# Kernel tuning notes

Hardware: AMD Instinct MI355X
Metric: run time of the kernel (lower is better)

Reference implementation:

```python
import jax, jax.numpy as jnp
import numpy as np

N = 20000      # nodes
E = 320000     # edges (avg degree 16)
F_IN = 32      # raw node feature dim
D = 128        # GNN_EMBEDDING_DIM = out_channels per head
HEADS = 4
RNN_H = 128    # RNN_HIDDEN_DIM
NEG_SLOPE = 0.2


def setup_inputs() -> dict:
    key = jax.random.key(0)
    ks = jax.random.split(key, 16)
    s = 0.05
    return {
        "node_features": jax.random.normal(ks[0], (N, F_IN), jnp.float32),
        "hidden_state": jax.random.normal(ks[1], (1, RNN_H), jnp.float32),
        "W_enc": jax.random.normal(ks[2], (F_IN, D), jnp.float32) * s,
        "b_enc": jax.random.normal(ks[3], (D,), jnp.float32) * s,
        "W_l": jax.random.normal(ks[4], (D, HEADS * D), jnp.float32) * s,
        "b_l": jax.random.normal(ks[5], (HEADS * D,), jnp.float32) * s,
        "W_r": jax.random.normal(ks[6], (D, HEADS * D), jnp.float32) * s,
        "b_r": jax.random.normal(ks[7], (HEADS * D,), jnp.float32) * s,
        "att": jax.random.normal(ks[8], (HEADS, D), jnp.float32) * s,
        "gat_bias": jax.random.normal(ks[9], (D,), jnp.float32) * s,
        "W_ih": jax.random.normal(ks[10], (3 * RNN_H, D), jnp.float32) * s,
        "W_hh": jax.random.normal(ks[11], (3 * RNN_H, RNN_H), jnp.float32) * s,
        "b_ih": jax.random.normal(ks[12], (3 * RNN_H,), jnp.float32) * s,
        "b_hh": jax.random.normal(ks[13], (3 * RNN_H,), jnp.float32) * s,
        "edge_index": jax.random.randint(ks[14], (2, E), 0, N, jnp.int32),
    }


def reference(node_features, hidden_state, W_enc, b_enc, W_l, b_l, W_r, b_r,
              att, gat_bias, W_ih, W_hh, b_ih, b_hh, edge_index):
    n = node_features.shape[0]
    # node encoder + ReLU
    h = jax.nn.relu(node_features @ W_enc + b_enc)                 # [N, D]

    # GATv2Conv (heads=4, concat=False), add_self_loops=True, eval (no dropout)
    loop = jnp.arange(n, dtype=edge_index.dtype)
    src = jnp.concatenate([edge_index[0], loop])                   # source j
    dst = jnp.concatenate([edge_index[1], loop])                   # target i

    xl = (h @ W_l + b_l).reshape(n, HEADS, D)                      # source proj
    xr = (h @ W_r + b_r).reshape(n, HEADS, D)                      # target proj

    e = jax.nn.leaky_relu(xl[src] + xr[dst], NEG_SLOPE)            # [Et, H, C]
    logits = jnp.einsum('ehc,hc->eh', e, att)                      # [Et, H]

    # segment softmax over incoming edges of each target node
    m = jax.ops.segment_max(logits, dst, num_segments=n)           # [N, H]
    m = jnp.where(jnp.isfinite(m), m, 0.0)
    p = jnp.exp(logits - m[dst])
    denom = jax.ops.segment_sum(p, dst, num_segments=n)
    alpha = p / jnp.maximum(denom[dst], 1e-16)                     # [Et, H]

    out = jax.ops.segment_sum(xl[src] * alpha[..., None], dst, num_segments=n)
    gat = out.mean(axis=1) + gat_bias                              # [N, D]

    # agent node 0 -> GRUCell (torch gate order: r, z, n)
    x = gat[0:1]                                                   # [1, D]
    gi = x @ W_ih.T + b_ih
    gh = hidden_state @ W_hh.T + b_hh
    i_r, i_z, i_n = jnp.split(gi, 3, axis=-1)
    h_r, h_z, h_n = jnp.split(gh, 3, axis=-1)
    r = jax.nn.sigmoid(i_r + h_r)
    z = jax.nn.sigmoid(i_z + h_z)
    ng = jnp.tanh(i_n + r * h_n)
    return (1.0 - z) * ng + z * hidden_state                       # [1, RNN_H]
```

## Files before the change

kernel.cpp:

```cpp
#include <hip/hip_runtime.h>


#define NBLK 40
#define NXL  16
#define XRB  16
#define GHB  24
#define FINB 36
#define SLOTS3 8
#define CAP  40
#define FLAGMAGIC 0x5A5A0000u

struct KP {
    const int* ei; int E;
    const float *nf, *W_enc, *b_enc, *W_l, *b_l, *W_r, *b_r, *att, *gat_bias,
                *hprev, *W_ih, *W_hh, *b_ih, *b_hh;
    unsigned *scnt;
    unsigned *xlflag;
    unsigned *xrflag;
    unsigned *gatflag;
    unsigned *giflag;
    int      *sslots;
    float *xr0;
    float *ghw;
    float *giw;
    float *gat;
    float *lgpart;
    float *xlw;
    float *out;
};

__device__ __forceinline__ unsigned pollFlag(unsigned* p) {
    for (long it = 0; it < 50000000L; ++it) {
        unsigned v = atomicOr(p, 0u);
        if ((v & 0xFFFF0000u) == FLAGMAGIC) return v & 0xFFFFu;
        __builtin_amdgcn_s_sleep(2);
    }
    return 0u;
}

__global__ __launch_bounds__(256) void k_all(KP p)
{
    __shared__ __align__(16) float buf[14720];
    __shared__ float aux[512];
    __shared__ int   iaux[128];
    const int t = threadIdx.x, b = blockIdx.x;

    if (t == 0) iaux[0] = 0;
    __syncthreads();
    if ((p.E & 3) == 0) {
        int nv = p.E >> 2;
        int per = (nv + NBLK - 1) / NBLK;
        int lo = b * per, hi = min(lo + per, nv);
        const int4* d4 = (const int4*)(p.ei + p.E);
        for (int it0 = lo; it0 < hi; it0 += 2048) {
            int4 v[8];
            #pragma unroll
            for (int k = 0; k < 8; ++k) {
                int i = it0 + t + k * 256;
                v[k] = (i < hi) ? d4[i] : make_int4(1, 1, 1, 1);
            }
            #pragma unroll
            for (int k = 0; k < 8; ++k) {
                int i = it0 + t + k * 256;
                if (v[k].x == 0 || v[k].y == 0 || v[k].z == 0 || v[k].w == 0) {
                    #pragma unroll
                    for (int c = 0; c < 4; ++c) {
                        if ((&v[k].x)[c] == 0) {
                            int q = atomicAdd(&iaux[0], 1);
                            if (q < SLOTS3) iaux[8 + q] = p.ei[4 * (long)i + c];
                        }
                    }
                }
            }
        }
    } else {
        int per = (p.E + NBLK - 1) / NBLK;
        long lo = (long)b * per, hi = lo + per; if (hi > p.E) hi = p.E;
        for (long i = lo + t; i < hi; i += 256) {
            if (p.ei[p.E + i] == 0) {
                int q = atomicAdd(&iaux[0], 1);
                if (q < SLOTS3) iaux[8 + q] = p.ei[i];
            }
        }
    }
    __syncthreads();
    int myc = min(iaux[0], SLOTS3);
    if (t < myc) p.sslots[b * SLOTS3 + t] = iaux[8 + t];
    __syncthreads();
    __threadfence();
    if (t == 0) atomicExch(&p.scnt[b * 16], FLAGMAGIC | (unsigned)myc);
    if (b > FINB) return;

    if (b >= XRB && b < GHB) {
        int q = b - XRB;
        for (int idx = t; idx < 2048; idx += 256) {
            int row = idx >> 4, f4 = idx & 15;
            ((float4*)buf)[idx] = *(const float4*)(p.W_r + (long)row * 512 + q * 64 + f4 * 4);
        }
        for (int idx = t; idx < 1024; idx += 256)
            ((float4*)(buf + 8192))[idx] = ((const float4*)p.W_enc)[idx];
        if (t < 32) aux[384 + t] = p.nf[t];
        __syncthreads();
        if (t < 128) {
            float a0 = 0, a1 = 0, a2 = 0, a3 = 0;
            #pragma unroll
            for (int k = 0; k < 32; k += 4) {
                a0 += aux[384 + k]     * buf[8192 + k * 128 + t];
                a1 += aux[384 + k + 1] * buf[8192 + (k + 1) * 128 + t];
                a2 += aux[384 + k + 2] * buf[8192 + (k + 2) * 128 + t];
                a3 += aux[384 + k + 3] * buf[8192 + (k + 3) * 128 + t];
            }
            aux[t] = fmaxf(a0 + a1 + a2 + a3 + p.b_enc[t], 0.f);
        }
        __syncthreads();
        {
            int jq = t & 63, ch = t >> 6;
            float a = 0.f;
            #pragma unroll 8
            for (int cc = 0; cc < 32; ++cc) {
                int c = ch * 32 + cc;
                a += aux[c] * buf[c * 64 + jq];
            }
            aux[128 + ch * 64 + jq] = a;
        }
        __syncthreads();
        if (t < 64) {
            int j = q * 64 + t;
            p.xr0[j] = aux[128 + t] + aux[192 + t] + aux[256 + t] + aux[320 + t]
                     + p.b_r[j];
        }
        __syncthreads();
        __threadfence();
        if (t == 0) atomicExch(&p.xrflag[q * 16], FLAGMAGIC | 1u);
        return;
    }

    if (b >= GHB && b < FINB) {
        int g = b - GHB;
        for (int idx = t; idx < 1024; idx += 256) {
            int row = idx >> 5, f4 = idx & 31;
            ((float4*)buf)[idx] = *(const float4*)(p.W_hh + (long)(g * 32 + row) * 128 + f4 * 4);
            ((float4*)(buf + 4096))[idx] = *(const float4*)(p.W_ih + (long)(g * 32 + row) * 128 + f4 * 4);
        }
        if (t < 128) aux[t] = p.hprev[t];
        __syncthreads();
        {
            int w = t >> 6, l = t & 63;
            #pragma unroll
            for (int i = 0; i < 8; ++i) {
                int rl = w * 8 + i;
                float pp = buf[rl * 128 + 2 * l] * aux[2 * l]
                         + buf[rl * 128 + 2 * l + 1] * aux[2 * l + 1];
                #pragma unroll
                for (int off = 32; off; off >>= 1) pp += __shfl_down(pp, off);
                if (l == 0) {
                    int r = g * 32 + rl;
                    p.ghw[r] = pp + p.b_hh[r];
                }
            }
        }
        if (t == 0) pollFlag(p.gatflag);
        __syncthreads();
        __threadfence();
        if (t < 128) aux[128 + t] = p.gat[t];
        __syncthreads();
        {
            int w = t >> 6, l = t & 63;
            #pragma unroll
            for (int i = 0; i < 8; ++i) {
                int rl = w * 8 + i;
                float pp = buf[4096 + rl * 128 + 2 * l] * aux[128 + 2 * l]
                         + buf[4096 + rl * 128 + 2 * l + 1] * aux[128 + 2 * l + 1];
                #pragma unroll
                for (int off = 32; off; off >>= 1) pp += __shfl_down(pp, off);
                if (l == 0) {
                    int r = g * 32 + rl;
                    p.giw[r] = pp + p.b_ih[r];
                }
            }
        }
        __syncthreads();
        __threadfence();
        if (t == 0) atomicExch(&p.giflag[g * 16], FLAGMAGIC | 1u);
        return;
    }

    if (b < NXL) {
        for (int idx = t; idx < 1024; idx += 256) {
            int row = idx >> 3, f4 = idx & 7;
            ((float4*)buf)[idx] = *(const float4*)(p.W_l + (long)row * 512 + b * 32 + f4 * 4);
        }
        for (int idx = t; idx < 1024; idx += 256)
            ((float4*)(buf + 4096))[idx] = ((const float4*)p.W_enc)[idx];

        if (t < NBLK) iaux[24 + t] = (int)pollFlag(&p.scnt[t * 16]);
        __syncthreads();
        __threadfence();
        if (t < 64) {
            int c = (t < NBLK) ? iaux[24 + t] : 0;
            int pre = c;
            #pragma unroll
            for (int off = 1; off < 64; off <<= 1) {
                int v = __shfl_up(pre, off);
                if (t >= off) pre += v;
            }
            int base = pre - c;
            for (int u = 0; u < c; ++u) {
                int pos = base + u;
                if (pos < CAP - 1) iaux[64 + pos] = p.sslots[t * SLOTS3 + u];
            }
            if (t == 63) iaux[1] = min(pre, CAP - 1);
        }
        __syncthreads();
        int Mc = iaux[1];
        if (t == 0) iaux[64 + Mc] = 0;
        __syncthreads();
        int Mt = Mc + 1;

        for (int idx = t; idx < Mt * 8; idx += 256) {
            int e = idx >> 3, f4 = idx & 7;
            ((float4*)(buf + 8192))[idx] = *(const float4*)(p.nf + (long)iaux[64 + e] * 32 + f4 * 4);
        }
        __syncthreads();
        {
            int eg = t >> 7, c = t & 127;
            for (int e = eg; e < Mt; e += 2) {
                float a0 = 0, a1 = 0, a2 = 0, a3 = 0;
                #pragma unroll
                for (int k = 0; k < 32; k += 4) {
                    a0 += buf[8192 + e * 32 + k]     * buf[4096 + k * 128 + c];
                    a1 += buf[8192 + e * 32 + k + 1] * buf[4096 + (k + 1) * 128 + c];
                    a2 += buf[8192 + e * 32 + k + 2] * buf[4096 + (k + 2) * 128 + c];
                    a3 += buf[8192 + e * 32 + k + 3] * buf[4096 + (k + 3) * 128 + c];
                }
                buf[9600 + e * 128 + c] = fmaxf(a0 + a1 + a2 + a3 + p.b_enc[c], 0.f);
            }
        }
        if (t == 0) pollFlag(&p.xrflag[(b >> 1) * 16]);
        __syncthreads();
        __threadfence();
        {
            int l5 = t & 31, hw = t >> 5;
            int j = b * 32 + l5;
            int ne = 0, el[5] = {0, 0, 0, 0, 0};
            for (int e = hw; e < Mt; e += 8) el[ne++] = e;
            float acc[5] = {0, 0, 0, 0, 0};
            #pragma unroll 4
            for (int c = 0; c < 128; ++c) {
                float wv = buf[c * 32 + l5];
                #pragma unroll
                for (int k = 0; k < 5; ++k)
                    if (k < ne) acc[k] += buf[9600 + el[k] * 128 + c] * wv;
            }
            float blj = p.b_l[j], xrj = p.xr0[j], atj = p.att[j];
            #pragma unroll
            for (int k = 0; k < 5; ++k) {
                if (k < ne) {
                    int e = el[k];
                    float xv = acc[k] + blj;
                    p.xlw[(long)e * 512 + j] = xv;
                    float v = xv + xrj;
                    v = (v > 0.f) ? v : 0.2f * v;
                    float pp = v * atj;
                    #pragma unroll
                    for (int off = 16; off; off >>= 1) pp += __shfl_down(pp, off, 32);
                    if (l5 == 0) aux[e] = pp;
                }
            }
        }
        __syncthreads();
        if (t < Mt) p.lgpart[b * CAP + t] = aux[t];
        __syncthreads();
        __threadfence();
        if (t == 0) atomicExch(&p.xlflag[b * 16], FLAGMAGIC | 1u);
        return;
    }

    if (t < NBLK) iaux[24 + t] = (int)pollFlag(&p.scnt[t * 16]);
    if (t >= 64 && t < 64 + NXL) pollFlag(&p.xlflag[(t - 64) * 16]);
    __syncthreads();
    __threadfence();
    if (t == 0) {
        int s = 0;
        for (int i = 0; i < NBLK; ++i) s += iaux[24 + i];
        iaux[1] = min(s, CAP - 1);
    }
    __syncthreads();
    int Mt = iaux[1] + 1;

    for (int idx = t; idx < NXL * CAP; idx += 256) buf[idx] = p.lgpart[idx];
    __syncthreads();
    if (t < 4) {
        int h = t;
        float m = -1e30f;
        for (int e = 0; e < Mt; ++e) {
            float lv = buf[(4 * h) * CAP + e] + buf[(4 * h + 1) * CAP + e]
                     + buf[(4 * h + 2) * CAP + e] + buf[(4 * h + 3) * CAP + e];
            buf[640 + e * 4 + h] = lv;
            m = fmaxf(m, lv);
        }
        float d = 0.f;
        for (int e = 0; e < Mt; ++e) d += expf(buf[640 + e * 4 + h] - m);
        float inv = 1.f / fmaxf(d, 1e-16f);
        for (int e = 0; e < Mt; ++e)
            buf[640 + e * 4 + h] = expf(buf[640 + e * 4 + h] - m) * inv;
    }
    __syncthreads();
    {
        #pragma unroll
        for (int jj = 0; jj < 2; ++jj) {
            int j = t + jj * 256, h = j >> 7;
            float a0 = 0, a1 = 0, a2 = 0, a3 = 0;
            int e = 0;
            for (; e + 3 < Mt; e += 4) {
                a0 += buf[640 + e * 4 + h]       * p.xlw[(long)e * 512 + j];
                a1 += buf[640 + (e + 1) * 4 + h] * p.xlw[(long)(e + 1) * 512 + j];
                a2 += buf[640 + (e + 2) * 4 + h] * p.xlw[(long)(e + 2) * 512 + j];
                a3 += buf[640 + (e + 3) * 4 + h] * p.xlw[(long)(e + 3) * 512 + j];
            }
            for (; e < Mt; ++e) a0 += buf[640 + e * 4 + h] * p.xlw[(long)e * 512 + j];
            buf[800 + j] = a0 + a1 + a2 + a3;
        }
    }
    __syncthreads();
    if (t < 128)
        p.gat[t] = 0.25f * (buf[800 + t] + buf[928 + t] + buf[1056 + t] + buf[1184 + t])
                 + p.gat_bias[t];
    __syncthreads();
    __threadfence();
    if (t == 0) atomicExch(p.gatflag, FLAGMAGIC | 1u);
    if (t < 12) pollFlag(&p.giflag[t * 16]);
    __syncthreads();
    __threadfence();
    if (t < 128) {
        float r = 1.f / (1.f + expf(-(p.giw[t] + p.ghw[t])));
        float z = 1.f / (1.f + expf(-(p.giw[128 + t] + p.ghw[128 + t])));
        float n = tanhf(p.giw[256 + t] + r * p.ghw[256 + t]);
        p.out[t] = (1.f - z) * n + z * p.hprev[t];
    }
}

extern "C" void kernel_launch(void* const* d_in, const int* in_sizes, int n_in,
                              void* d_out, int out_size, void* d_ws, size_t ws_size,
                              hipStream_t stream) {
    KP kp;
    kp.nf       = (const float*)d_in[0];
    kp.hprev    = (const float*)d_in[1];
    kp.W_enc    = (const float*)d_in[2];
    kp.b_enc    = (const float*)d_in[3];
    kp.W_l      = (const float*)d_in[4];
    kp.b_l      = (const float*)d_in[5];
    kp.W_r      = (const float*)d_in[6];
    kp.b_r      = (const float*)d_in[7];
    kp.att      = (const float*)d_in[8];
    kp.gat_bias = (const float*)d_in[9];
    kp.W_ih     = (const float*)d_in[10];
    kp.W_hh     = (const float*)d_in[11];
    kp.b_ih     = (const float*)d_in[12];
    kp.b_hh     = (const float*)d_in[13];
    kp.ei       = (const int*)d_in[14];
    kp.E = in_sizes[14] / 2;

    char* ws = (char*)d_ws;
    kp.scnt    = (unsigned*)(ws + 0);
    kp.xlflag  = (unsigned*)(ws + 2560);
    kp.xrflag  = (unsigned*)(ws + 3584);
    kp.gatflag = (unsigned*)(ws + 4096);
    kp.giflag  = (unsigned*)(ws + 4160);
    kp.sslots  = (int*)(ws + 4928);
    kp.xr0     = (float*)(ws + 6272);
    kp.ghw     = (float*)(ws + 8320);
    kp.giw     = (float*)(ws + 9856);
    kp.gat     = (float*)(ws + 11392);
    kp.lgpart  = (float*)(ws + 11904);
    kp.xlw     = (float*)(ws + 14464);
    kp.out     = (float*)d_out;

    k_all<<<NBLK, 256, 0, stream>>>(kp);
}
```

Before: 124.6 us.

## Restructure fused GAT+GRU kernel to 28 blocks with fewer cross-block handoffs

Shrinks the persistent grid from 40 to 28 blocks and drops the separate xr0 and GRU-hidden blocks. Each xl block now computes its own xr slice and keeps xl in shared memory, then does the softmax and weighted sum locally and publishes a per-head partial output. The 12 GRU blocks each compute a row chunk of both gate matrices and the final output, removing the single finalizer block and the gat/gi flag round trips. The scan of edge targets for node 0 now uses fewer blocks with deeper per-thread unrolling, so each block streams more data.

Result: faster. 114.3 us (-8.3%).

```diff
diff --git a/kernel.cpp b/kernel.cpp
--- a/kernel.cpp
+++ b/kernel.cpp
@@ -1,11 +1,10 @@
 #include <hip/hip_runtime.h>
 
 
-#define NBLK 40
+#define NBLK 28
 #define NXL  16
-#define XRB  16
-#define GHB  24
-#define FINB 36
+#define NGT  12
+#define NCH  11
 #define SLOTS3 8
 #define CAP  40
 #define FLAGMAGIC 0x5A5A0000u
@@ -16,16 +15,10 @@
                 *hprev, *W_ih, *W_hh, *b_ih, *b_hh;
     unsigned *scnt;
     unsigned *xlflag;
-    unsigned *xrflag;
-    unsigned *gatflag;
-    unsigned *giflag;
+    unsigned *o0flag;
     int      *sslots;
-    float *xr0;
-    float *ghw;
-    float *giw;
-    float *gat;
     float *lgpart;
-    float *xlw;
+    float *out0;
     float *out;
 };
 
@@ -38,6 +31,8 @@
     return 0u;
 }
 
+__device__ __forceinline__ float sigm(float x) { return 1.f / (1.f + expf(-x)); }
+
 __global__ __launch_bounds__(256) void k_all(KP p)
 {
     __shared__ __align__(16) float buf[14720];
@@ -52,16 +47,16 @@
         int per = (nv + NBLK - 1) / NBLK;
         int lo = b * per, hi = min(lo + per, nv);
         const int4* d4 = (const int4*)(p.ei + p.E);
-        for (int it0 = lo; it0 < hi; it0 += 2048) {
-            int4 v[8];
-            #pragma unroll
-            for (int k = 0; k < 8; ++k) {
-                int i = it0 + t + k * 256;
+        for (int base = lo; base < hi; base += 256 * 12) {
+            int4 v[12];
+            #pragma unroll
+            for (int k = 0; k < 12; ++k) {
+                int i = base + t + k * 256;
                 v[k] = (i < hi) ? d4[i] : make_int4(1, 1, 1, 1);
             }
             #pragma unroll
-            for (int k = 0; k < 8; ++k) {
-                int i = it0 + t + k * 256;
+            for (int k = 0; k < 12; ++k) {
+                int i = base + t + k * 256;
                 if (v[k].x == 0 || v[k].y == 0 || v[k].z == 0 || v[k].w == 0) {
                     #pragma unroll
                     for (int c = 0; c < 4; ++c) {
@@ -89,103 +84,12 @@
     __syncthreads();
     __threadfence();
     if (t == 0) atomicExch(&p.scnt[b * 16], FLAGMAGIC | (unsigned)myc);
-    if (b > FINB) return;
-
-    if (b >= XRB && b < GHB) {
-        int q = b - XRB;
-        for (int idx = t; idx < 2048; idx += 256) {
-            int row = idx >> 4, f4 = idx & 15;
-            ((float4*)buf)[idx] = *(const float4*)(p.W_r + (long)row * 512 + q * 64 + f4 * 4);
-        }
-        for (int idx = t; idx < 1024; idx += 256)
-            ((float4*)(buf + 8192))[idx] = ((const float4*)p.W_enc)[idx];
-        if (t < 32) aux[384 + t] = p.nf[t];
-        __syncthreads();
-        if (t < 128) {
-            float a0 = 0, a1 = 0, a2 = 0, a3 = 0;
-            #pragma unroll
-            for (int k = 0; k < 32; k += 4) {
-                a0 += aux[384 + k]     * buf[8192 + k * 128 + t];
-                a1 += aux[384 + k + 1] * buf[8192 + (k + 1) * 128 + t];
-                a2 += aux[384 + k + 2] * buf[8192 + (k + 2) * 128 + t];
-                a3 += aux[384 + k + 3] * buf[8192 + (k + 3) * 128 + t];
-            }
-            aux[t] = fmaxf(a0 + a1 + a2 + a3 + p.b_enc[t], 0.f);
-        }
-        __syncthreads();
-        {
-            int jq = t & 63, ch = t >> 6;
-            float a = 0.f;
-            #pragma unroll 8
-            for (int cc = 0; cc < 32; ++cc) {
-                int c = ch * 32 + cc;
-                a += aux[c] * buf[c * 64 + jq];
-            }
-            aux[128 + ch * 64 + jq] = a;
-        }
-        __syncthreads();
-        if (t < 64) {
-            int j = q * 64 + t;
-            p.xr0[j] = aux[128 + t] + aux[192 + t] + aux[256 + t] + aux[320 + t]
-                     + p.b_r[j];
-        }
-        __syncthreads();
-        __threadfence();
-        if (t == 0) atomicExch(&p.xrflag[q * 16], FLAGMAGIC | 1u);
-        return;
-    }
-
-    if (b >= GHB && b < FINB) {
-        int g = b - GHB;
-        for (int idx = t; idx < 1024; idx += 256) {
-            int row = idx >> 5, f4 = idx & 31;
-            ((float4*)buf)[idx] = *(const float4*)(p.W_hh + (long)(g * 32 + row) * 128 + f4 * 4);
-            ((float4*)(buf + 4096))[idx] = *(const float4*)(p.W_ih + (long)(g * 32 + row) * 128 + f4 * 4);
-        }
-        if (t < 128) aux[t] = p.hprev[t];
-        __syncthreads();
-        {
-            int w = t >> 6, l = t & 63;
-            #pragma unroll
-            for (int i = 0; i < 8; ++i) {
-                int rl = w * 8 + i;
-                float pp = buf[rl * 128 + 2 * l] * aux[2 * l]
-                         + buf[rl * 128 + 2 * l + 1] * aux[2 * l + 1];
-                #pragma unroll
-                for (int off = 32; off; off >>= 1) pp += __shfl_down(pp, off);
-                if (l == 0) {
-                    int r = g * 32 + rl;
-                    p.ghw[r] = pp + p.b_hh[r];
-                }
-            }
-        }
-        if (t == 0) pollFlag(p.gatflag);
-        __syncthreads();
-        __threadfence();
-        if (t < 128) aux[128 + t] = p.gat[t];
-        __syncthreads();
-        {
-            int w = t >> 6, l = t & 63;
-            #pragma unroll
-            for (int i = 0; i < 8; ++i) {
-                int rl = w * 8 + i;
-                float pp = buf[4096 + rl * 128 + 2 * l] * aux[128 + 2 * l]
-                         + buf[4096 + rl * 128 + 2 * l + 1] * aux[128 + 2 * l + 1];
-                #pragma unroll
-                for (int off = 32; off; off >>= 1) pp += __shfl_down(pp, off);
-                if (l == 0) {
-                    int r = g * 32 + rl;
-                    p.giw[r] = pp + p.b_ih[r];
-                }
-            }
-        }
-        __syncthreads();
-        __threadfence();
-        if (t == 0) atomicExch(&p.giflag[g * 16], FLAGMAGIC | 1u);
-        return;
-    }
 
     if (b < NXL) {
+        const int l5 = t & 31, hw = t >> 5;
+        const int j = b * 32 + l5;
+        float blv = p.b_l[j], atv = p.att[j];
+        float brv = (t < 32) ? p.b_r[b * 32 + t] : 0.f;
         for (int idx = t; idx < 1024; idx += 256) {
             int row = idx >> 3, f4 = idx & 7;
             ((float4*)buf)[idx] = *(const float4*)(p.W_l + (long)row * 512 + b * 32 + f4 * 4);
@@ -193,11 +97,11 @@
         for (int idx = t; idx < 1024; idx += 256)
             ((float4*)(buf + 4096))[idx] = ((const float4*)p.W_enc)[idx];
 
-        if (t < NBLK) iaux[24 + t] = (int)pollFlag(&p.scnt[t * 16]);
+        if (t < NBLK) iaux[32 + t] = (int)pollFlag(&p.scnt[t * 16]);
         __syncthreads();
         __threadfence();
         if (t < 64) {
-            int c = (t < NBLK) ? iaux[24 + t] : 0;
+            int c = (t < NBLK) ? iaux[32 + t] : 0;
             int pre = c;
             #pragma unroll
             for (int off = 1; off < 64; off <<= 1) {
@@ -236,32 +140,51 @@
                 buf[9600 + e * 128 + c] = fmaxf(a0 + a1 + a2 + a3 + p.b_enc[c], 0.f);
             }
         }
-        if (t == 0) pollFlag(&p.xrflag[(b >> 1) * 16]);
-        __syncthreads();
-        __threadfence();
+        __syncthreads();
+        for (int idx = t; idx < 1024; idx += 256) {
+            int row = idx >> 3, f4 = idx & 7;
+            ((float4*)(buf + 4096))[idx] = *(const float4*)(p.W_r + (long)row * 512 + b * 32 + f4 * 4);
+        }
+        __syncthreads();
+        if (t < 32) {
+            float s0 = 0, s1 = 0, s2 = 0, s3 = 0;
+            const float* h0 = &buf[9600 + (Mt - 1) * 128];
+            #pragma unroll 8
+            for (int c = 0; c < 128; c += 4) {
+                s0 += h0[c]     * buf[4096 + c * 32 + t];
+                s1 += h0[c + 1] * buf[4096 + (c + 1) * 32 + t];
+                s2 += h0[c + 2] * buf[4096 + (c + 2) * 32 + t];
+                s3 += h0[c + 3] * buf[4096 + (c + 3) * 32 + t];
+            }
+            aux[192 + t] = s0 + s1 + s2 + s3 + brv;
+        }
+        int ne = 0, el[5] = {0, 0, 0, 0, 0};
+        for (int e = hw; e < Mt; e += 8) el[ne++] = e;
+        float acc[5] = {0, 0, 0, 0, 0};
+        #pragma unroll 4
+        for (int c = 0; c < 128; c += 4) {
+            float w0 = buf[c * 32 + l5],       w1 = buf[(c + 1) * 32 + l5];
+            float w2 = buf[(c + 2) * 32 + l5], w3 = buf[(c + 3) * 32 + l5];
+            #pragma unroll
+            for (int k = 0; k < 5; ++k) {
+                if (k < ne) {
+                    float4 h4 = *(const float4*)&buf[9600 + el[k] * 128 + c];
+                    acc[k] += h4.x * w0 + h4.y * w1 + h4.z * w2 + h4.w * w3;
+                }
+            }
+        }
+        __syncthreads();
         {
-            int l5 = t & 31, hw = t >> 5;
-            int j = b * 32 + l5;
-            int ne = 0, el[5] = {0, 0, 0, 0, 0};
-            for (int e = hw; e < Mt; e += 8) el[ne++] = e;
-            float acc[5] = {0, 0, 0, 0, 0};
-            #pragma unroll 4
-            for (int c = 0; c < 128; ++c) {
-                float wv = buf[c * 32 + l5];
-                #pragma unroll
-                for (int k = 0; k < 5; ++k)
-                    if (k < ne) acc[k] += buf[9600 + el[k] * 128 + c] * wv;
-            }
-            float blj = p.b_l[j], xrj = p.xr0[j], atj = p.att[j];
+            float xrj = aux[192 + l5];
             #pragma unroll
             for (int k = 0; k < 5; ++k) {
                 if (k < ne) {
                     int e = el[k];
-                    float xv = acc[k] + blj;
-                    p.xlw[(long)e * 512 + j] = xv;
+                    float xv = acc[k] + blv;
+                    buf[8192 + e * 32 + l5] = xv;
                     float v = xv + xrj;
                     v = (v > 0.f) ? v : 0.2f * v;
-                    float pp = v * atj;
+                    float pp = v * atv;
                     #pragma unroll
                     for (int off = 16; off; off >>= 1) pp += __shfl_down(pp, off, 32);
                     if (l5 == 0) aux[e] = pp;
@@ -273,70 +196,96 @@
         __syncthreads();
         __threadfence();
         if (t == 0) atomicExch(&p.xlflag[b * 16], FLAGMAGIC | 1u);
+
+        if (t < NXL) pollFlag(&p.xlflag[t * 16]);
+        __syncthreads();
+        __threadfence();
+        for (int idx = t; idx < NXL * CAP; idx += 256)
+            buf[idx] = p.lgpart[idx];
+        __syncthreads();
+        if (t < 4) {
+            int h = t;
+            float m = -1e30f;
+            for (int e = 0; e < Mt; ++e) {
+                float lv = buf[(4 * h) * CAP + e] + buf[(4 * h + 1) * CAP + e]
+                         + buf[(4 * h + 2) * CAP + e] + buf[(4 * h + 3) * CAP + e];
+                aux[256 + e * 4 + h] = lv;
+                m = fmaxf(m, lv);
+            }
+            float d = 0.f;
+            for (int e = 0; e < Mt; ++e) d += expf(aux[256 + e * 4 + h] - m);
+            float inv = 1.f / fmaxf(d, 1e-16f);
+            for (int e = 0; e < Mt; ++e)
+                aux[256 + e * 4 + h] = expf(aux[256 + e * 4 + h] - m) * inv;
+        }
+        __syncthreads();
+        if (t < 32) {
+            int h = b >> 2;
+            float s = 0.f;
+            for (int e = 0; e < Mt; ++e)
+                s += aux[256 + e * 4 + h] * buf[8192 + e * 32 + t];
+            p.out0[b * 32 + t] = s;
+        }
+        __syncthreads();
+        __threadfence();
+        if (t == 0) atomicExch(&p.o0flag[b * 16], FLAGMAGIC | 1u);
         return;
     }
 
-    if (t < NBLK) iaux[24 + t] = (int)pollFlag(&p.scnt[t * 16]);
-    if (t >= 64 && t < 64 + NXL) pollFlag(&p.xlflag[(t - 64) * 16]);
-    __syncthreads();
-    __threadfence();
-    if (t == 0) {
-        int s = 0;
-        for (int i = 0; i < NBLK; ++i) s += iaux[24 + i];
-        iaux[1] = min(s, CAP - 1);
-    }
-    __syncthreads();
-    int Mt = iaux[1] + 1;
-
-    for (int idx = t; idx < NXL * CAP; idx += 256) buf[idx] = p.lgpart[idx];
-    __syncthreads();
-    if (t < 4) {
-        int h = t;
-        float m = -1e30f;
-        for (int e = 0; e < Mt; ++e) {
-            float lv = buf[(4 * h) * CAP + e] + buf[(4 * h + 1) * CAP + e]
-                     + buf[(4 * h + 2) * CAP + e] + buf[(4 * h + 3) * CAP + e];
-            buf[640 + e * 4 + h] = lv;
-            m = fmaxf(m, lv);
-        }
-        float d = 0.f;
-        for (int e = 0; e < Mt; ++e) d += expf(buf[640 + e * 4 + h] - m);
-        float inv = 1.f / fmaxf(d, 1e-16f);
-        for (int e = 0; e < Mt; ++e)
-            buf[640 + e * 4 + h] = expf(buf[640 + e * 4 + h] - m) * inv;
-    }
-    __syncthreads();
     {
-        #pragma unroll
-        for (int jj = 0; jj < 2; ++jj) {
-            int j = t + jj * 256, h = j >> 7;
-            float a0 = 0, a1 = 0, a2 = 0, a3 = 0;
-            int e = 0;
-            for (; e + 3 < Mt; e += 4) {
-                a0 += buf[640 + e * 4 + h]       * p.xlw[(long)e * 512 + j];
-                a1 += buf[640 + (e + 1) * 4 + h] * p.xlw[(long)(e + 1) * 512 + j];
-                a2 += buf[640 + (e + 2) * 4 + h] * p.xlw[(long)(e + 2) * 512 + j];
-                a3 += buf[640 + (e + 3) * 4 + h] * p.xlw[(long)(e + 3) * 512 + j];
-            }
-            for (; e < Mt; ++e) a0 += buf[640 + e * 4 + h] * p.xlw[(long)e * 512 + j];
-            buf[800 + j] = a0 + a1 + a2 + a3;
-        }
-    }
-    __syncthreads();
-    if (t < 128)
-        p.gat[t] = 0.25f * (buf[800 + t] + buf[928 + t] + buf[1056 + t] + buf[1184 + t])
-                 + p.gat_bias[t];
-    __syncthreads();
-    __threadfence();
-    if (t == 0) atomicExch(p.gatflag, FLAGMAGIC | 1u);
-    if (t < 12) pollFlag(&p.giflag[t * 16]);
-    __syncthreads();
-    __threadfence();
-    if (t < 128) {
-        float r = 1.f / (1.f + expf(-(p.giw[t] + p.ghw[t])));
-        float z = 1.f / (1.f + expf(-(p.giw[128 + t] + p.ghw[128 + t])));
-        float n = tanhf(p.giw[256 + t] + r * p.ghw[256 + t]);
-        p.out[t] = (1.f - z) * n + z * p.hprev[t];
+        int g = b - NXL;
+        int nch = min(NCH, 128 - g * NCH);
+        if (t < 128) aux[256 + t] = p.hprev[t];
+        for (int idx = t; idx < 6 * NCH * 32; idx += 256) {
+            int chunk = idx / (NCH * 32);
+            int rin = (idx % (NCH * 32)) >> 5;
+            int f4 = idx & 31;
+            if (rin < nch) {
+                int grow = (chunk % 3) * 128 + g * NCH + rin;
+                const float* W = (chunk < 3) ? p.W_ih : p.W_hh;
+                ((float4*)buf)[idx] = *(const float4*)(W + (long)grow * 128 + f4 * 4);
+            }
+        }
+        __syncthreads();
+        {
+            int w = t >> 6, l = t & 63;
+            for (int rr = w; rr < 3 * nch; rr += 4) {
+                int gate = rr / nch, rin = rr % nch;
+                int chunk = 3 + gate;
+                float2 wv = ((const float2*)&buf[chunk * (NCH * 128) + rin * 128])[l];
+                float pp = wv.x * aux[256 + 2 * l] + wv.y * aux[256 + 2 * l + 1];
+                #pragma unroll
+                for (int off = 32; off; off >>= 1) pp += __shfl_down(pp, off);
+                if (l == 0) aux[rr] = pp + p.b_hh[gate * 128 + g * NCH + rin];
+            }
+        }
+        if (t < NXL) pollFlag(&p.o0flag[t * 16]);
+        __syncthreads();
+        __threadfence();
+        if (t < 128)
+            aux[384 + t] = 0.25f * (p.out0[t] + p.out0[128 + t] +
+                                    p.out0[256 + t] + p.out0[384 + t])
+                         + p.gat_bias[t];
+        __syncthreads();
+        {
+            int w = t >> 6, l = t & 63;
+            for (int rr = w; rr < 3 * nch; rr += 4) {
+                int gate = rr / nch, rin = rr % nch;
+                float2 wv = ((const float2*)&buf[gate * (NCH * 128) + rin * 128])[l];
+                float pp = wv.x * aux[384 + 2 * l] + wv.y * aux[384 + 2 * l + 1];
+                #pragma unroll
+                for (int off = 32; off; off >>= 1) pp += __shfl_down(pp, off);
+                if (l == 0) aux[64 + rr] = pp + p.b_ih[gate * 128 + g * NCH + rin];
+            }
+        }
+        __syncthreads();
+        if (t < nch) {
+            int c = g * NCH + t;
+            float r = sigm(aux[64 + t]           + aux[t]);
+            float z = sigm(aux[64 + nch + t]     + aux[nch + t]);
+            float n = tanhf(aux[64 + 2 * nch + t] + r * aux[2 * nch + t]);
+            p.out[c] = (1.f - z) * n + z * aux[256 + c];
+        }
     }
 }
 
@@ -362,19 +311,13 @@
     kp.E = in_sizes[14] / 2;
 
     char* ws = (char*)d_ws;
-    kp.scnt    = (unsigned*)(ws + 0);
-    kp.xlflag  = (unsigned*)(ws + 2560);
-    kp.xrflag  = (unsigned*)(ws + 3584);
-    kp.gatflag = (unsigned*)(ws + 4096);
-    kp.giflag  = (unsigned*)(ws + 4160);
-    kp.sslots  = (int*)(ws + 4928);
-    kp.xr0     = (float*)(ws + 6272);
-    kp.ghw     = (float*)(ws + 8320);
-    kp.giw     = (float*)(ws + 9856);
-    kp.gat     = (float*)(ws + 11392);
-    kp.lgpart  = (float*)(ws + 11904);
-    kp.xlw     = (float*)(ws + 14464);
-    kp.out     = (float*)d_out;
+    kp.scnt   = (unsigned*)(ws + 0);
+    kp.xlflag = (unsigned*)(ws + 1792);
+    kp.o0flag = (unsigned*)(ws + 2816);
+    kp.sslots = (int*)(ws + 3840);
+    kp.lgpart = (float*)(ws + 4736);
+    kp.out0   = (float*)(ws + 7296);
+    kp.out    = (float*)d_out;
 
     k_all<<<NBLK, 256, 0, stream>>>(kp);
 }
```
